# Kernel optimization log

Measured on AMD Instinct MI355X. Metric: run time of the kernel, lower is better.

## Reference

```python
import jax, jax.numpy as jnp
import numpy as np

N = 100_000      # nodes
E = 1_600_000    # edges
EL = 200_000     # labeled edge pairs
NODE_DIM, HID = 32, 256
H2, H4 = HID // 2, HID // 4  # 128, 64


def _lin(k, fan_in, fan_out):
    kw, kb = jax.random.split(k)
    bound = 1.0 / np.sqrt(fan_in)
    W = jax.random.uniform(kw, (fan_in, fan_out), jnp.float32, -bound, bound)
    b = jax.random.uniform(kb, (fan_out,), jnp.float32, -bound, bound)
    return W, b


def setup_inputs() -> dict:
    key = jax.random.key(0)
    ks = jax.random.split(key, 12)
    x = jax.random.normal(ks[0], (N, NODE_DIM), jnp.float32)
    edge_index = jax.random.randint(ks[1], (2, E), 0, N, jnp.int64)
    edge_label_index = jax.random.randint(ks[2], (2, EL), 0, N, jnp.int64)
    enc_w1, enc_b1 = _lin(ks[3], NODE_DIM, HID)
    enc_w2, enc_b2 = _lin(ks[4], HID, H2)
    conv_w0, conv_b0 = _lin(ks[5], H2, H4)
    conv_w1, conv_b1 = _lin(ks[6], H4, H4)
    conv_w2, conv_b2 = _lin(ks[7], H4, H4)
    ep_w1, ep_b1 = _lin(ks[8], 2 * H4, H2)
    ep_w2, ep_b2 = _lin(ks[9], H2, H4)
    ep_w3, ep_b3 = _lin(ks[10], H4, 1)
    return dict(x=x, edge_index=edge_index, edge_label_index=edge_label_index,
                enc_w1=enc_w1, enc_b1=enc_b1, enc_w2=enc_w2, enc_b2=enc_b2,
                conv_w0=conv_w0, conv_b0=conv_b0, conv_w1=conv_w1, conv_b1=conv_b1,
                conv_w2=conv_w2, conv_b2=conv_b2,
                ep_w1=ep_w1, ep_b1=ep_b1, ep_w2=ep_w2, ep_b2=ep_b2, ep_w3=ep_w3, ep_b3=ep_b3)


def reference(x, edge_index, edge_label_index,
              enc_w1, enc_b1, enc_w2, enc_b2,
              conv_w0, conv_b0, conv_w1, conv_b1, conv_w2, conv_b2,
              ep_w1, ep_b1, ep_w2, ep_b2, ep_w3, ep_b3):
    # node encoder (dropout = identity in eval)
    h = jax.nn.relu(x @ enc_w1 + enc_b1)
    h = jax.nn.relu(h @ enc_w2 + enc_b2)           # [N, 128]

    # GCN normalization with self-loops (PyG gcn_norm, edge_weight=1)
    loops = jnp.arange(N, dtype=edge_index.dtype)
    src = jnp.concatenate([edge_index[0], loops])   # [E+N]
    dst = jnp.concatenate([edge_index[1], loops])
    deg = jax.ops.segment_sum(jnp.ones(E + N, jnp.float32), dst, num_segments=N)
    dinv = jnp.where(deg > 0, jax.lax.rsqrt(jnp.maximum(deg, 1.0)), 0.0)
    norm = (dinv[src] * dinv[dst])[:, None]          # [E+N, 1]

    def gcn(h, W, b):
        xw = h @ W                                   # transform first (PyG)
        agg = jax.ops.segment_sum(xw[src] * norm, dst, num_segments=N)
        return agg + b

    for W, b in ((conv_w0, conv_b0), (conv_w1, conv_b1), (conv_w2, conv_b2)):
        h_new = jax.nn.relu(gcn(h, W, b))
        h = h + h_new if h.shape == h_new.shape else h_new
        # self.dropout -> identity in eval

    # edge predictor on labeled pairs
    ef = jnp.concatenate([h[edge_label_index[0]], h[edge_label_index[1]]], axis=1)  # [EL, 128]
    e = jax.nn.relu(ef @ ep_w1 + ep_b1)
    e = jax.nn.relu(e @ ep_w2 + ep_b2)
    e = jax.nn.sigmoid(e @ ep_w3 + ep_b3)
    return e.squeeze(-1)                             # [EL]
```

## Files before the change

kernel.cpp:

```cpp
#include <hip/hip_runtime.h>
#include <math.h>


#define N_NODES 100000
#define N_EDGES 1600000
#define N_EL    200000

#define KBUCK   196
#define WSHIFT  9
#define WMASK   511
#define BCAP    64
#define BSTRIDE 12288
#define PART_NB 512
#define CHUNK   3125
#define LCAP    10240
#define ENC_NB  1563

typedef __attribute__((ext_vector_type(8))) short short8_t;
typedef __attribute__((ext_vector_type(4))) float f32x4;

__device__ __forceinline__ unsigned short f2bf(float f) {
    unsigned u = __float_as_uint(f);
    unsigned r = u + 0x7FFFu + ((u >> 16) & 1u);
    return (unsigned short)(r >> 16);
}

__device__ __forceinline__ float2 up16(unsigned u) {
    union { unsigned v; _Float16 h[2]; } c; c.v = u;
    return make_float2((float)c.h[0], (float)c.h[1]);
}

template<int KTOT, int NTOT>
__device__ __forceinline__ void wprep_one(const float* __restrict__ W, unsigned short* __restrict__ Wp, int flat) {
    if (flat >= KTOT * NTOT) return;
    int j = flat & 7, lane = (flat >> 3) & 63, kstep = (flat >> 9) & 1;
    int rest = flat >> 10;
    int ntile = rest % (NTOT / 16), chunk = rest / (NTOT / 16);
    int k = chunk * 64 + kstep * 32 + (lane >> 4) * 8 + j;
    int n = ntile * 16 + (lane & 15);
    Wp[flat] = f2bf(W[(size_t)k * NTOT + n]);
}

__device__ __forceinline__ void wprep32_one(const float* __restrict__ W, unsigned short* __restrict__ Wp, int flat) {
    if (flat >= 32 * 256) return;
    int j = flat & 7, lane = (flat >> 3) & 63, ntile = flat >> 9;
    int k = (lane >> 4) * 8 + j;
    int n = ntile * 16 + (lane & 15);
    Wp[flat] = f2bf(W[(size_t)k * 256 + n]);
}

__global__ __launch_bounds__(256) void prep0(
    const float* w2, const float* w0, const float* w1, const float* wpp2, const float* w1e,
    const float* wc1, const float* wc2,
    unsigned short* p2, unsigned short* p0, unsigned short* p1, unsigned short* pp2,
    unsigned short* p1e, unsigned short* pc1, unsigned short* pc2,
    int* btail)
{
    int blk = blockIdx.x, t = threadIdx.x;
    if      (blk < 128) wprep_one<256, 128>(w2,  p2,  blk * 256 + t);
    else if (blk < 160) wprep_one<128,  64>(w0,  p0,  (blk - 128) * 256 + t);
    else if (blk < 224) wprep_one<128, 128>(w1,  p1,  (blk - 160) * 256 + t);
    else if (blk < 256) wprep_one<128,  64>(wpp2, pp2, (blk - 224) * 256 + t);
    else if (blk < 288) wprep32_one(w1e, p1e, (blk - 256) * 256 + t);
    else if (blk < 304) wprep_one< 64,  64>(wc1, pc1, (blk - 288) * 256 + t);
    else if (blk < 320) wprep_one< 64,  64>(wc2, pc2, (blk - 304) * 256 + t);
    else                btail[t] = 0;
}

__device__ __forceinline__ void fill_part_body(unsigned char* sm,
                                               const int* __restrict__ ei,
                                               int* __restrict__ btail, int* __restrict__ bscr)
{
    int* base = (int*)sm;
    int (*lbuf)[BCAP] = (int(*)[BCAP])base;
    int* lcnt  = base + 12544;
    int* offs  = base + 12740;
    int* gbase = base + 12937;
    int* sscan = base + 13133;
    int t = threadIdx.x;

    for (int i = t; i < KBUCK; i += 256) lcnt[i] = 0;
    __syncthreads();

    int e0   = blockIdx.x * CHUNK;
    int eend = e0 + CHUNK; if (eend > N_EDGES) eend = N_EDGES;
    for (int e = e0 + t; e < eend; e += 256) {
        int s = __builtin_nontemporal_load(ei + e);
        int d = __builtin_nontemporal_load(ei + N_EDGES + e);
        int b = d >> WSHIFT;
        int entry = ((d & WMASK) << 17) | s;
        int pos = atomicAdd(&lcnt[b], 1);
        if (pos < BCAP) lbuf[b][pos] = entry;
        else {
            int p = atomicAdd(&btail[b], 1);
            bscr[b * BSTRIDE + p] = entry;
        }
    }
    __syncthreads();

    int myc = 0;
    if (t < KBUCK) {
        myc = lcnt[t]; if (myc > BCAP) myc = BCAP;
        lcnt[t] = myc;
        gbase[t] = atomicAdd(&btail[t], myc);
    }
    sscan[t] = (t < KBUCK) ? myc : 0;
    __syncthreads();
    for (int s = 1; s < 256; s <<= 1) {
        int a = (t >= s) ? sscan[t - s] : 0;
        __syncthreads();
        sscan[t] += a;
        __syncthreads();
    }
    if (t < KBUCK) offs[t + 1] = sscan[t];
    if (t == 0) offs[0] = 0;
    __syncthreads();

    int T = offs[KBUCK];
    for (int i = t; i < T; i += 256) {
        int loB = 0, hiB = KBUCK;
        while (hiB - loB > 1) { int mid = (loB + hiB) >> 1; if (offs[mid] <= i) loB = mid; else hiB = mid; }
        int j = i - offs[loB];
        bscr[loB * BSTRIDE + gbase[loB] + j] = lbuf[loB][j];
    }
}

__device__ __forceinline__ void encfull_body(unsigned char* sm, int bid,
    const float* __restrict__ x,
    const unsigned short* __restrict__ Wp1, const float* __restrict__ b1,
    const unsigned short* __restrict__ Wp2, const float* __restrict__ b2,
    const unsigned short* __restrict__ Wp0,
    _Float16* __restrict__ yout, int M)
{
    unsigned short* smem = (unsigned short*)sm;
    unsigned short (*As)[40]   = (unsigned short(*)[40])smem;
    unsigned short* Wls1       = smem + 2560;
    unsigned short (*H1)[264]  = (unsigned short(*)[264])smem;
    unsigned short (*H128)[136]= (unsigned short(*)[136])smem;
    unsigned short* Wls2       = smem + 16896;
    unsigned short* W0s        = smem + 16896;

    int t = threadIdx.x, wave = t >> 6, lane = t & 63;
    int m0 = bid * 64;
    int cb = lane & 15, rq = lane >> 4;

    {
        int row = t >> 2, seg = t & 3;
        int gr = m0 + row;
        float4 a = make_float4(0.f, 0.f, 0.f, 0.f), b = a;
        if (gr < M) {
            a = *(const float4*)&x[(size_t)gr * 32 + seg * 8];
            b = *(const float4*)&x[(size_t)gr * 32 + seg * 8 + 4];
        }
        unsigned short tmp[8] = { f2bf(a.x), f2bf(a.y), f2bf(a.z), f2bf(a.w),
                                  f2bf(b.x), f2bf(b.y), f2bf(b.z), f2bf(b.w) };
        *(uint4*)&As[row][seg * 8] = *(uint4*)tmp;
    }
    #pragma unroll
    for (int j = 0; j < 4; ++j)
        ((uint4*)Wls1)[t + j * 256] = ((const uint4*)Wp1)[t + j * 256];
    __syncthreads();

    short8_t af1 = *(const short8_t*)&As[wave * 16 + cb][rq * 8];
    f32x4 acc[16];
    #pragma unroll
    for (int nt = 0; nt < 16; ++nt) {
        short8_t bf = *(const short8_t*)&Wls1[(nt * 64 + lane) * 8];
        acc[nt] = __builtin_amdgcn_mfma_f32_16x16x32_bf16(af1, bf, (f32x4){0.f, 0.f, 0.f, 0.f}, 0, 0, 0);
    }
    __syncthreads();

    #pragma unroll
    for (int nt = 0; nt < 16; ++nt) {
        int col = nt * 16 + cb;
        float bv = b1[col];
        #pragma unroll
        for (int r = 0; r < 4; ++r)
            H1[wave * 16 + rq * 4 + r][col] = f2bf(fmaxf(acc[nt][r] + bv, 0.f));
    }

    f32x4 acc2[8];
    #pragma unroll
    for (int nt = 0; nt < 8; ++nt) acc2[nt] = (f32x4){0.f, 0.f, 0.f, 0.f};
    for (int ch = 0; ch < 4; ++ch) {
        #pragma unroll
        for (int j = 0; j < 4; ++j)
            ((uint4*)Wls2)[t + j * 256] = ((const uint4*)(Wp2 + (size_t)ch * 8192))[t + j * 256];
        __syncthreads();
        #pragma unroll
        for (int ks = 0; ks < 2; ++ks) {
            short8_t af = *(const short8_t*)&H1[wave * 16 + cb][ch * 64 + ks * 32 + rq * 8];
            #pragma unroll
            for (int nt = 0; nt < 8; ++nt) {
                short8_t bf = *(const short8_t*)&Wls2[((nt * 2 + ks) * 64 + lane) * 8];
                acc2[nt] = __builtin_amdgcn_mfma_f32_16x16x32_bf16(af, bf, acc2[nt], 0, 0, 0);
            }
        }
        __syncthreads();
    }

    #pragma unroll
    for (int nt = 0; nt < 8; ++nt) {
        int col = nt * 16 + cb;
        float bv = b2[col];
        #pragma unroll
        for (int r = 0; r < 4; ++r)
            H128[wave * 16 + rq * 4 + r][col] = f2bf(fmaxf(acc2[nt][r] + bv, 0.f));
    }
    ((uint4*)W0s)[t]       = ((const uint4*)Wp0)[t];
    ((uint4*)W0s)[t + 256] = ((const uint4*)Wp0)[t + 256];
    __syncthreads();

    f32x4 acc3[4];
    #pragma unroll
    for (int nt = 0; nt < 4; ++nt) acc3[nt] = (f32x4){0.f, 0.f, 0.f, 0.f};
    #pragma unroll
    for (int ch = 0; ch < 2; ++ch) {
        #pragma unroll
        for (int ks = 0; ks < 2; ++ks) {
            short8_t af = *(const short8_t*)&H128[wave * 16 + cb][ch * 64 + ks * 32 + rq * 8];
            #pragma unroll
            for (int nt = 0; nt < 4; ++nt) {
                short8_t bf = *(const short8_t*)&W0s[(((ch * 4 + nt) * 2 + ks) * 64 + lane) * 8];
                acc3[nt] = __builtin_amdgcn_mfma_f32_16x16x32_bf16(af, bf, acc3[nt], 0, 0, 0);
            }
        }
    }

    #pragma unroll
    for (int nt = 0; nt < 4; ++nt) {
        int col = nt * 16 + cb;
        #pragma unroll
        for (int r = 0; r < 4; ++r) {
            int gr = m0 + wave * 16 + rq * 4 + r;
            if (gr < M) yout[(size_t)gr * 64 + col] = (_Float16)(acc3[nt][r]);
        }
    }
}

__global__ __launch_bounds__(256, 3) void mega_fill_enc(
    const int* __restrict__ ei, int* __restrict__ btail, int* __restrict__ bscr,
    const float* __restrict__ x,
    const unsigned short* __restrict__ Wp1, const float* __restrict__ b1,
    const unsigned short* __restrict__ Wp2, const float* __restrict__ b2,
    const unsigned short* __restrict__ Wp0,
    _Float16* __restrict__ yout)
{
    __shared__ __align__(16) unsigned char sm[53568];
    if (blockIdx.x < PART_NB)
        fill_part_body(sm, ei, btail, bscr);
    else
        encfull_body(sm, blockIdx.x - PART_NB, x, Wp1, b1, Wp2, b2, Wp0, yout, N_NODES);
}

__global__ __launch_bounds__(512) void fill_place(const int* __restrict__ btail,
                                                  const int* __restrict__ bscr,
                                                  int* __restrict__ row_ptr, float* __restrict__ dinv,
                                                  int* __restrict__ col) {
    __shared__ int ssm[256];
    __shared__ int lcnt[512];
    __shared__ int lpre[512];
    __shared__ int lbuf[LCAP];
    int b = blockIdx.x, t = threadIdx.x;

    if (t < 256) ssm[t] = (t < KBUCK) ? btail[t] : 0;
    lcnt[t] = 0;
    __syncthreads();
    for (int s = 1; s < 256; s <<= 1) {
        int a = 0;
        if (t < 256 && t >= s) a = ssm[t - s];
        __syncthreads();
        if (t < 256) ssm[t] += a;
        __syncthreads();
    }
    int segstart = (b == 0) ? 0 : ssm[b - 1];
    int n = btail[b];
    const int* src = bscr + b * BSTRIDE;
    for (int i = t; i < n; i += 512)
        atomicAdd(&lcnt[src[i] >> 17], 1);
    __syncthreads();

    int c = lcnt[t];
    lpre[t] = c; __syncthreads();
    for (int s = 1; s < 512; s <<= 1) {
        int a = (t >= s) ? lpre[t - s] : 0;
        __syncthreads();
        lpre[t] += a;
        __syncthreads();
    }
    int excl = lpre[t] - c;

    int v = (b << WSHIFT) + t;
    if (v < N_NODES) {
        row_ptr[v] = segstart + excl;
        dinv[v] = rsqrtf((float)(c + 1));
    }
    if (b == KBUCK - 1 && t == 0) row_ptr[N_NODES] = N_EDGES;
    lcnt[t] = excl;
    __syncthreads();

    if (n <= LCAP) {
        for (int i = t; i < n; i += 512) {
            int e = src[i];
            int pos = atomicAdd(&lcnt[e >> 17], 1);
            lbuf[pos] = e & 0x1FFFF;
        }
        __syncthreads();
        for (int i = t; i < n; i += 512)
            col[segstart + i] = lbuf[i];
    } else {
        for (int i = t; i < n; i += 512) {
            int e = src[i];
            int pos = atomicAdd(&lcnt[e >> 17], 1);
            col[segstart + pos] = e & 0x1FFFF;
        }
    }
}

template<bool RESIDUAL, bool EDGE_DINV>
__device__ __forceinline__ void aggcv_body(
    const uint4* __restrict__ y4, const int* __restrict__ row_ptr, const int* __restrict__ col,
    const float* __restrict__ dinv, const float* __restrict__ bias,
    const unsigned short* __restrict__ Wp,
    _Float16* __restrict__ h,
    _Float16* __restrict__ yout)
{
    __shared__ __align__(16) unsigned short Ws[4096];
    __shared__ __align__(16) unsigned short Hs[32][72];
    __shared__ float Dv[32];

    int t = threadIdx.x;
    ((uint4*)Ws)[t]       = ((const uint4*)Wp)[t];
    ((uint4*)Ws)[t + 256] = ((const uint4*)Wp)[t + 256];

    int n  = t >> 3;
    int sl = t & 7;
    int v  = blockIdx.x * 32 + n;

    float dv = dinv[v];

    float s[8];
    {
        uint4 a = y4[(size_t)v * 8 + sl];
        float2 g;
        float w = EDGE_DINV ? dv : 1.0f;
        if (EDGE_DINV) {
            g = up16(a.x); s[0] = w * g.x; s[1] = w * g.y;  g = up16(a.y); s[2] = w * g.x; s[3] = w * g.y;
            g = up16(a.z); s[4] = w * g.x; s[5] = w * g.y;  g = up16(a.w); s[6] = w * g.x; s[7] = w * g.y;
        } else {
            g = up16(a.x); s[0] = g.x; s[1] = g.y;  g = up16(a.y); s[2] = g.x; s[3] = g.y;
            g = up16(a.z); s[4] = g.x; s[5] = g.y;  g = up16(a.w); s[6] = g.x; s[7] = g.y;
        }
    }
    auto accrow = [&](uint4 f, float w) {
        float2 g;
        if (EDGE_DINV) {
            g = up16(f.x); s[0] += w * g.x; s[1] += w * g.y;  g = up16(f.y); s[2] += w * g.x; s[3] += w * g.y;
            g = up16(f.z); s[4] += w * g.x; s[5] += w * g.y;  g = up16(f.w); s[6] += w * g.x; s[7] += w * g.y;
        } else {
            g = up16(f.x); s[0] += g.x; s[1] += g.y;  g = up16(f.y); s[2] += g.x; s[3] += g.y;
            g = up16(f.z); s[4] += g.x; s[5] += g.y;  g = up16(f.w); s[6] += g.x; s[7] += g.y;
        }
    };

    int rs = row_ptr[v], re = row_ptr[v + 1];
    int i = rs;
    for (; i + 7 < re; i += 8) {
        int u0 = col[i],     u1 = col[i + 1], u2 = col[i + 2], u3 = col[i + 3];
        int u4 = col[i + 4], u5 = col[i + 5], u6 = col[i + 6], u7 = col[i + 7];
        float d0 = EDGE_DINV ? dinv[u0] : 1.0f, d1 = EDGE_DINV ? dinv[u1] : 1.0f;
        float d2 = EDGE_DINV ? dinv[u2] : 1.0f, d3 = EDGE_DINV ? dinv[u3] : 1.0f;
        float d4 = EDGE_DINV ? dinv[u4] : 1.0f, d5 = EDGE_DINV ? dinv[u5] : 1.0f;
        float d6 = EDGE_DINV ? dinv[u6] : 1.0f, d7 = EDGE_DINV ? dinv[u7] : 1.0f;
        uint4 f0 = y4[(size_t)u0 * 8 + sl];
        uint4 f1 = y4[(size_t)u1 * 8 + sl];
        uint4 f2 = y4[(size_t)u2 * 8 + sl];
        uint4 f3 = y4[(size_t)u3 * 8 + sl];
        uint4 f4 = y4[(size_t)u4 * 8 + sl];
        uint4 f5 = y4[(size_t)u5 * 8 + sl];
        uint4 f6 = y4[(size_t)u6 * 8 + sl];
        uint4 f7 = y4[(size_t)u7 * 8 + sl];
        accrow(f0, d0); accrow(f1, d1); accrow(f2, d2); accrow(f3, d3);
        accrow(f4, d4); accrow(f5, d5); accrow(f6, d6); accrow(f7, d7);
    }
    for (; i + 3 < re; i += 4) {
        int u0 = col[i], u1 = col[i + 1], u2 = col[i + 2], u3 = col[i + 3];
        float d0 = EDGE_DINV ? dinv[u0] : 1.0f, d1 = EDGE_DINV ? dinv[u1] : 1.0f;
        float d2 = EDGE_DINV ? dinv[u2] : 1.0f, d3 = EDGE_DINV ? dinv[u3] : 1.0f;
        uint4 f0 = y4[(size_t)u0 * 8 + sl];
        uint4 f1 = y4[(size_t)u1 * 8 + sl];
        uint4 f2 = y4[(size_t)u2 * 8 + sl];
        uint4 f3 = y4[(size_t)u3 * 8 + sl];
        accrow(f0, d0); accrow(f1, d1); accrow(f2, d2); accrow(f3, d3);
    }
    for (; i < re; ++i) {
        int u = col[i];
        float d = EDGE_DINV ? dinv[u] : 1.0f;
        accrow(y4[(size_t)u * 8 + sl], d);
    }

    float4 ba = *(const float4*)&bias[sl * 8];
    float4 bb = *(const float4*)&bias[sl * 8 + 4];
    float v0 = fmaxf(dv * s[0] + ba.x, 0.f), v1 = fmaxf(dv * s[1] + ba.y, 0.f);
    float v2 = fmaxf(dv * s[2] + ba.z, 0.f), v3 = fmaxf(dv * s[3] + ba.w, 0.f);
    float v4 = fmaxf(dv * s[4] + bb.x, 0.f), v5 = fmaxf(dv * s[5] + bb.y, 0.f);
    float v6 = fmaxf(dv * s[6] + bb.z, 0.f), v7 = fmaxf(dv * s[7] + bb.w, 0.f);
    if (RESIDUAL) {
        uint4 hr = *(const uint4*)&h[(size_t)v * 64 + sl * 8];
        float2 g;
        g = up16(hr.x); v0 += g.x; v1 += g.y;  g = up16(hr.y); v2 += g.x; v3 += g.y;
        g = up16(hr.z); v4 += g.x; v5 += g.y;  g = up16(hr.w); v6 += g.x; v7 += g.y;
    }
    union { _Float16 hf[8]; uint4 u; } hp;
    hp.hf[0] = (_Float16)v0; hp.hf[1] = (_Float16)v1; hp.hf[2] = (_Float16)v2; hp.hf[3] = (_Float16)v3;
    hp.hf[4] = (_Float16)v4; hp.hf[5] = (_Float16)v5; hp.hf[6] = (_Float16)v6; hp.hf[7] = (_Float16)v7;
    *(uint4*)&h[(size_t)v * 64 + sl * 8] = hp.u;
    union { unsigned short us[8]; uint4 u; } hb;
    hb.us[0] = f2bf(v0); hb.us[1] = f2bf(v1); hb.us[2] = f2bf(v2); hb.us[3] = f2bf(v3);
    hb.us[4] = f2bf(v4); hb.us[5] = f2bf(v5); hb.us[6] = f2bf(v6); hb.us[7] = f2bf(v7);
    *(uint4*)&Hs[n][sl * 8] = hb.u;
    if (sl == 0) Dv[n] = dv;
    __syncthreads();

    int wave = t >> 6, lane = t & 63;
    int rt   = wave & 1;
    int ct0  = (wave >> 1) * 2;
    f32x4 acc0 = (f32x4){0.f, 0.f, 0.f, 0.f}, acc1 = acc0;
    #pragma unroll
    for (int ks = 0; ks < 2; ++ks) {
        short8_t af = *(const short8_t*)&Hs[rt * 16 + (lane & 15)][ks * 32 + (lane >> 4) * 8];
        short8_t b0 = *(const short8_t*)&Ws[((ct0 * 2 + ks) * 64 + lane) * 8];
        short8_t b1 = *(const short8_t*)&Ws[(((ct0 + 1) * 2 + ks) * 64 + lane) * 8];
        acc0 = __builtin_amdgcn_mfma_f32_16x16x32_bf16(af, b0, acc0, 0, 0, 0);
        acc1 = __builtin_amdgcn_mfma_f32_16x16x32_bf16(af, b1, acc1, 0, 0, 0);
    }
    int cb = lane & 15, rq = lane >> 4;
    #pragma unroll
    for (int r = 0; r < 4; ++r) {
        int row = rt * 16 + rq * 4 + r;
        float dv2 = Dv[row];
        size_t go = (size_t)(blockIdx.x * 32 + row) * 64;
        yout[go + ct0 * 16 + cb]       = (_Float16)(acc0[r] * dv2);
        yout[go + (ct0 + 1) * 16 + cb] = (_Float16)(acc1[r] * dv2);
    }
}

__global__ __launch_bounds__(256, 6) void aggcv0_kernel(
    const uint4* y, const int* rp, const int* col, const float* dinv, const float* b,
    const unsigned short* Wp, _Float16* h, _Float16* yout) {
    aggcv_body<false, true>(y, rp, col, dinv, b, Wp, h, yout);
}
__global__ __launch_bounds__(256, 6) void aggcv1_kernel(
    const uint4* y, const int* rp, const int* col, const float* dinv, const float* b,
    const unsigned short* Wp, _Float16* h, _Float16* yout) {
    aggcv_body<true, false>(y, rp, col, dinv, b, Wp, h, yout);
}

__global__ __launch_bounds__(256, 6) void agg2_kernel(
    const uint4* __restrict__ y4, const int* __restrict__ row_ptr, const int* __restrict__ col,
    const float* __restrict__ dinv, const float* __restrict__ bias,
    const _Float16* __restrict__ hprev, uint4* __restrict__ hb4)
{
    int v  = blockIdx.x * 32 + (threadIdx.x >> 3);
    int sl = threadIdx.x & 7;
    if (v >= N_NODES) return;

    float s[8];
    {
        uint4 a = y4[(size_t)v * 8 + sl];
        float2 g;
        g = up16(a.x); s[0] = g.x; s[1] = g.y;  g = up16(a.y); s[2] = g.x; s[3] = g.y;
        g = up16(a.z); s[4] = g.x; s[5] = g.y;  g = up16(a.w); s[6] = g.x; s[7] = g.y;
    }
    auto accrow = [&](uint4 f) {
        float2 g;
        g = up16(f.x); s[0] += g.x; s[1] += g.y;  g = up16(f.y); s[2] += g.x; s[3] += g.y;
        g = up16(f.z); s[4] += g.x; s[5] += g.y;  g = up16(f.w); s[6] += g.x; s[7] += g.y;
    };

    int rs = row_ptr[v], re = row_ptr[v + 1];
    int i = rs;
    for (; i + 7 < re; i += 8) {
        int u0 = col[i],     u1 = col[i + 1], u2 = col[i + 2], u3 = col[i + 3];
        int u4 = col[i + 4], u5 = col[i + 5], u6 = col[i + 6], u7 = col[i + 7];
        uint4 f0 = y4[(size_t)u0 * 8 + sl];
        uint4 f1 = y4[(size_t)u1 * 8 + sl];
        uint4 f2 = y4[(size_t)u2 * 8 + sl];
        uint4 f3 = y4[(size_t)u3 * 8 + sl];
        uint4 f4 = y4[(size_t)u4 * 8 + sl];
        uint4 f5 = y4[(size_t)u5 * 8 + sl];
        uint4 f6 = y4[(size_t)u6 * 8 + sl];
        uint4 f7 = y4[(size_t)u7 * 8 + sl];
        accrow(f0); accrow(f1); accrow(f2); accrow(f3);
        accrow(f4); accrow(f5); accrow(f6); accrow(f7);
    }
    for (; i + 3 < re; i += 4) {
        int u0 = col[i], u1 = col[i + 1], u2 = col[i + 2], u3 = col[i + 3];
        uint4 f0 = y4[(size_t)u0 * 8 + sl];
        uint4 f1 = y4[(size_t)u1 * 8 + sl];
        uint4 f2 = y4[(size_t)u2 * 8 + sl];
        uint4 f3 = y4[(size_t)u3 * 8 + sl];
        accrow(f0); accrow(f1); accrow(f2); accrow(f3);
    }
    for (; i < re; ++i) accrow(y4[(size_t)col[i] * 8 + sl]);

    float dv = dinv[v];
    float4 ba = *(const float4*)&bias[sl * 8];
    float4 bb = *(const float4*)&bias[sl * 8 + 4];
    float v0 = fmaxf(dv * s[0] + ba.x, 0.f), v1 = fmaxf(dv * s[1] + ba.y, 0.f);
    float v2 = fmaxf(dv * s[2] + ba.z, 0.f), v3 = fmaxf(dv * s[3] + ba.w, 0.f);
    float v4 = fmaxf(dv * s[4] + bb.x, 0.f), v5 = fmaxf(dv * s[5] + bb.y, 0.f);
    float v6 = fmaxf(dv * s[6] + bb.z, 0.f), v7 = fmaxf(dv * s[7] + bb.w, 0.f);
    {
        uint4 hr = *(const uint4*)&hprev[(size_t)v * 64 + sl * 8];
        float2 g;
        g = up16(hr.x); v0 += g.x; v1 += g.y;  g = up16(hr.y); v2 += g.x; v3 += g.y;
        g = up16(hr.z); v4 += g.x; v5 += g.y;  g = up16(hr.w); v6 += g.x; v7 += g.y;
    }
    uint4 p;
    p.x = (unsigned)f2bf(v0) | ((unsigned)f2bf(v1) << 16);
    p.y = (unsigned)f2bf(v2) | ((unsigned)f2bf(v3) << 16);
    p.z = (unsigned)f2bf(v4) | ((unsigned)f2bf(v5) << 16);
    p.w = (unsigned)f2bf(v6) | ((unsigned)f2bf(v7) << 16);
    hb4[(size_t)v * 8 + sl] = p;
}

__global__ __launch_bounds__(256, 4) void mfma_ep12(
    const unsigned short* __restrict__ A, const int* __restrict__ gidx,
    const unsigned short* __restrict__ Wp1, const float* __restrict__ b1,
    const unsigned short* __restrict__ Wp2, const float* __restrict__ b2,
    const float* __restrict__ w3, const float* __restrict__ b3,
    float* __restrict__ out, int M)
{
    __shared__ __align__(16) unsigned short smem[12800];
    unsigned short (*As)[72] = (unsigned short(*)[72])smem;
    unsigned short* Wls = smem + 4608;

    int t = threadIdx.x, wave = t >> 6, lane = t & 63;
    int m0 = blockIdx.x * 64;
    int cb = lane & 15, rq = lane >> 4;

    f32x4 acc[8];
    #pragma unroll
    for (int nt = 0; nt < 8; ++nt) acc[nt] = (f32x4){0.f, 0.f, 0.f, 0.f};

    for (int ch = 0; ch < 2; ++ch) {
        #pragma unroll
        for (int j = 0; j < 2; ++j) {
            int idx = t + j * 256;
            int row = idx >> 3, seg = idx & 7;
            int gr = m0 + row;
            uint4 v = make_uint4(0u, 0u, 0u, 0u);
            if (gr < M) {
                int node = (ch == 0) ? gidx[gr] : gidx[N_EL + gr];
                v = *(const uint4*)(A + (size_t)node * 64 + seg * 8);
            }
            *(uint4*)&As[row][seg * 8] = v;
        }
        #pragma unroll
        for (int j = 0; j < 4; ++j) {
            int idx = t + j * 256;
            ((uint4*)Wls)[idx] = ((const uint4*)(Wp1 + (size_t)ch * 8192))[idx];
        }
        __syncthreads();

        #pragma unroll
        for (int ks = 0; ks < 2; ++ks) {
            short8_t af = *(const short8_t*)&As[wave * 16 + cb][ks * 32 + rq * 8];
            #pragma unroll
            for (int nt = 0; nt < 8; ++nt) {
                short8_t bf = *(const short8_t*)&Wls[((nt * 2 + ks) * 64 + lane) * 8];
                acc[nt] = __builtin_amdgcn_mfma_f32_16x16x32_bf16(af, bf, acc[nt], 0, 0, 0);
            }
        }
        __syncthreads();
    }

    unsigned short (*E1)[136] = (unsigned short(*)[136])smem;
    unsigned short* W2s = smem + 8704;
    #pragma unroll
    for (int nt = 0; nt < 8; ++nt) {
        int col = nt * 16 + cb;
        float bv = b1[col];
        #pragma unroll
        for (int r = 0; r < 4; ++r) {
            int row = wave * 16 + rq * 4 + r;
            E1[row][col] = f2bf(fmaxf(acc[nt][r] + bv, 0.f));
        }
    }
    ((uint4*)W2s)[t]       = ((const uint4*)Wp2)[t];
    ((uint4*)W2s)[t + 256] = ((const uint4*)Wp2)[t + 256];
    __syncthreads();

    f32x4 acc2[4];
    #pragma unroll
    for (int nt = 0; nt < 4; ++nt) acc2[nt] = (f32x4){0.f, 0.f, 0.f, 0.f};
    #pragma unroll
    for (int ch = 0; ch < 2; ++ch) {
        #pragma unroll
        for (int ks = 0; ks < 2; ++ks) {
            short8_t af = *(const short8_t*)&E1[wave * 16 + cb][ch * 64 + ks * 32 + rq * 8];
            #pragma unroll
            for (int nt = 0; nt < 4; ++nt) {
                short8_t bf = *(const short8_t*)&W2s[(((ch * 4 + nt) * 2 + ks) * 64 + lane) * 8];
                acc2[nt] = __builtin_amdgcn_mfma_f32_16x16x32_bf16(af, bf, acc2[nt], 0, 0, 0);
            }
        }
    }

    float s0 = 0.f, s1 = 0.f, s2 = 0.f, s3 = 0.f;
    #pragma unroll
    for (int nt = 0; nt < 4; ++nt) {
        int col = nt * 16 + cb;
        float bv = b2[col], wv = w3[col];
        s0 += fmaxf(acc2[nt][0] + bv, 0.f) * wv;
        s1 += fmaxf(acc2[nt][1] + bv, 0.f) * wv;
        s2 += fmaxf(acc2[nt][2] + bv, 0.f) * wv;
        s3 += fmaxf(acc2[nt][3] + bv, 0.f) * wv;
    }
    #pragma unroll
    for (int off = 1; off < 16; off <<= 1) {
        s0 += __shfl_xor(s0, off);
        s1 += __shfl_xor(s1, off);
        s2 += __shfl_xor(s2, off);
        s3 += __shfl_xor(s3, off);
    }
    if (cb == 0) {
        int gr = m0 + wave * 16 + rq * 4;
        if (gr + 3 < M) {
            float bb = b3[0];
            float4 o;
            o.x = 1.f / (1.f + expf(-(s0 + bb)));
            o.y = 1.f / (1.f + expf(-(s1 + bb)));
            o.z = 1.f / (1.f + expf(-(s2 + bb)));
            o.w = 1.f / (1.f + expf(-(s3 + bb)));
            *(float4*)&out[gr] = o;
        }
    }
}

extern "C" void kernel_launch(void* const* d_in, const int* in_sizes, int n_in,
                              void* d_out, int out_size, void* d_ws, size_t ws_size,
                              hipStream_t stream) {
    const float* x       = (const float*)d_in[0];
    const int*   ei      = (const int*)d_in[1];
    const int*   eli     = (const int*)d_in[2];
    const float* enc_w1  = (const float*)d_in[3];
    const float* enc_b1  = (const float*)d_in[4];
    const float* enc_w2  = (const float*)d_in[5];
    const float* enc_b2  = (const float*)d_in[6];
    const float* conv_w0 = (const float*)d_in[7];
    const float* conv_b0 = (const float*)d_in[8];
    const float* conv_w1 = (const float*)d_in[9];
    const float* conv_b1 = (const float*)d_in[10];
    const float* conv_w2 = (const float*)d_in[11];
    const float* conv_b2 = (const float*)d_in[12];
    const float* ep_w1   = (const float*)d_in[13];
    const float* ep_b1   = (const float*)d_in[14];
    const float* ep_w2   = (const float*)d_in[15];
    const float* ep_b2   = (const float*)d_in[16];
    const float* ep_w3   = (const float*)d_in[17];
    const float* ep_b3   = (const float*)d_in[18];
    float* out = (float*)d_out;

    float* fws = (float*)d_ws;
    _Float16* yb         = (_Float16*)fws;
    _Float16* h16        = (_Float16*)(fws + 3200000);
    unsigned short* h64b = (unsigned short*)(fws + 9600000);
    int*   col     = (int*)(fws + 12800000);
    int*   row_ptr = col + 1600000;
    float* dinvp   = (float*)(row_ptr + 100032);
    unsigned short* w2p = (unsigned short*)(dinvp + 100000);
    unsigned short* w0p = w2p + 32768;
    unsigned short* w1p = w0p + 8192;
    unsigned short* wp2 = w1p + 16384;
    unsigned short* w1e = wp2 + 8192;
    unsigned short* wc1p = w1e + 8192;
    unsigned short* wc2p = wc1p + 4096;
    int*   btail   = (int*)(wc2p + 4096);
    int*   bscr    = btail + 256;

    _Float16* yb2 = (_Float16*)h64b;

    const int GBE = N_EL / 64;
    const int GBA = N_NODES / 32;

    prep0<<<321, 256, 0, stream>>>(enc_w2, conv_w0, ep_w1, ep_w2, enc_w1, conv_w1, conv_w2,
                                   w2p, w0p, w1p, wp2, w1e, wc1p, wc2p, btail);

    mega_fill_enc<<<PART_NB + ENC_NB, 256, 0, stream>>>(ei, btail, bscr,
        x, w1e, enc_b1, w2p, enc_b2, w0p, yb);

    fill_place<<<KBUCK, 512, 0, stream>>>(btail, bscr, row_ptr, dinvp, col);

    aggcv0_kernel<<<GBA, 256, 0, stream>>>((const uint4*)yb, row_ptr, col, dinvp, conv_b0,
                                           wc1p, h16, yb2);
    aggcv1_kernel<<<GBA, 256, 0, stream>>>((const uint4*)yb2, row_ptr, col, dinvp, conv_b1,
                                           wc2p, h16, yb);
    agg2_kernel<<<GBA, 256, 0, stream>>>((const uint4*)yb, row_ptr, col, dinvp, conv_b2,
                                         h16, (uint4*)h64b);

    mfma_ep12<<<GBE, 256, 0, stream>>>(h64b, eli, w1p, ep_b1, wp2, ep_b2, ep_w3, ep_b3, out, N_EL);
}
```

Measured before the change: 273.3 us.

## Co-schedule CSR place stage with encoder instead of partition stage

The edge partition step becomes its own kernel, and the CSR placement step (rewritten for 256 threads, two nodes per thread) is fused into the same launch as the node encoder. The placement work now overlaps the encoder instead of the partition work doing so. The longer placement blocks may hide better behind the encoder and the launch count stays the same. The costs are a smaller placement block, which means more per-thread serial work, and a standalone partition kernel that no longer overlaps anything.

```diff
diff --git a/kernel.cpp b/kernel.cpp
--- a/kernel.cpp
+++ b/kernel.cpp
@@ -67,10 +67,10 @@
     else                btail[t] = 0;
 }
 
-__device__ __forceinline__ void fill_part_body(unsigned char* sm,
-                                               const int* __restrict__ ei,
-                                               int* __restrict__ btail, int* __restrict__ bscr)
+__global__ __launch_bounds__(256) void fill_part(const int* __restrict__ ei,
+                                                 int* __restrict__ btail, int* __restrict__ bscr)
 {
+    __shared__ __align__(16) unsigned char sm[53568];
     int* base = (int*)sm;
     int (*lbuf)[BCAP] = (int(*)[BCAP])base;
     int* lcnt  = base + 12544;
@@ -122,6 +122,77 @@
         while (hiB - loB > 1) { int mid = (loB + hiB) >> 1; if (offs[mid] <= i) loB = mid; else hiB = mid; }
         int j = i - offs[loB];
         bscr[loB * BSTRIDE + gbase[loB] + j] = lbuf[loB][j];
+    }
+}
+
+__device__ __forceinline__ void fill_place_body256(unsigned char* sm, int b,
+    const int* __restrict__ btail, const int* __restrict__ bscr,
+    int* __restrict__ row_ptr, float* __restrict__ dinv, int* __restrict__ col)
+{
+    int* base = (int*)sm;
+    int* ssm  = base;
+    int* lcnt = base + 256;
+    int* lpre = base + 768;
+    int* lbuf = base + 1024;
+    int t = threadIdx.x;
+
+    ssm[t] = (t < KBUCK) ? btail[t] : 0;
+    lcnt[t] = 0; lcnt[t + 256] = 0;
+    __syncthreads();
+    for (int s = 1; s < 256; s <<= 1) {
+        int a = (t >= s) ? ssm[t - s] : 0;
+        __syncthreads();
+        ssm[t] += a;
+        __syncthreads();
+    }
+    int segstart = (b == 0) ? 0 : ssm[b - 1];
+    int n = btail[b];
+    const int* src = bscr + b * BSTRIDE;
+    for (int i = t; i < n; i += 256)
+        atomicAdd(&lcnt[src[i] >> 17], 1);
+    __syncthreads();
+
+    int c0 = lcnt[2 * t], c1 = lcnt[2 * t + 1];
+    int cs = c0 + c1;
+    lpre[t] = cs; __syncthreads();
+    for (int s = 1; s < 256; s <<= 1) {
+        int a = (t >= s) ? lpre[t - s] : 0;
+        __syncthreads();
+        lpre[t] += a;
+        __syncthreads();
+    }
+    int exclp = lpre[t] - cs;
+    int excl0 = exclp, excl1 = exclp + c0;
+
+    int v0 = (b << WSHIFT) + 2 * t;
+    if (v0 < N_NODES) {
+        row_ptr[v0] = segstart + excl0;
+        dinv[v0] = rsqrtf((float)(c0 + 1));
+    }
+    if (v0 + 1 < N_NODES) {
+        row_ptr[v0 + 1] = segstart + excl1;
+        dinv[v0 + 1] = rsqrtf((float)(c1 + 1));
+    }
+    if (b == KBUCK - 1 && t == 0) row_ptr[N_NODES] = N_EDGES;
+    lcnt[2 * t] = excl0;
+    lcnt[2 * t + 1] = excl1;
+    __syncthreads();
+
+    if (n <= LCAP) {
+        for (int i = t; i < n; i += 256) {
+            int e = src[i];
+            int pos = atomicAdd(&lcnt[e >> 17], 1);
+            lbuf[pos] = e & 0x1FFFF;
+        }
+        __syncthreads();
+        for (int i = t; i < n; i += 256)
+            col[segstart + i] = lbuf[i];
+    } else {
+        for (int i = t; i < n; i += 256) {
+            int e = src[i];
+            int pos = atomicAdd(&lcnt[e >> 17], 1);
+            col[segstart + pos] = e & 0x1FFFF;
+        }
     }
 }
 
@@ -238,83 +309,20 @@
     }
 }
 
-__global__ __launch_bounds__(256, 3) void mega_fill_enc(
-    const int* __restrict__ ei, int* __restrict__ btail, int* __restrict__ bscr,
+__global__ __launch_bounds__(256, 3) void mega_place_enc(
+    const int* __restrict__ btail, const int* __restrict__ bscr,
+    int* __restrict__ row_ptr, float* __restrict__ dinv, int* __restrict__ col,
     const float* __restrict__ x,
     const unsigned short* __restrict__ Wp1, const float* __restrict__ b1,
     const unsigned short* __restrict__ Wp2, const float* __restrict__ b2,
     const unsigned short* __restrict__ Wp0,
     _Float16* __restrict__ yout)
 {
-    __shared__ __align__(16) unsigned char sm[53568];
-    if (blockIdx.x < PART_NB)
-        fill_part_body(sm, ei, btail, bscr);
+    __shared__ __align__(16) unsigned char sm[50176];
+    if (blockIdx.x < KBUCK)
+        fill_place_body256(sm, blockIdx.x, btail, bscr, row_ptr, dinv, col);
     else
-        encfull_body(sm, blockIdx.x - PART_NB, x, Wp1, b1, Wp2, b2, Wp0, yout, N_NODES);
-}
-
-__global__ __launch_bounds__(512) void fill_place(const int* __restrict__ btail,
-                                                  const int* __restrict__ bscr,
-                                                  int* __restrict__ row_ptr, float* __restrict__ dinv,
-                                                  int* __restrict__ col) {
-    __shared__ int ssm[256];
-    __shared__ int lcnt[512];
-    __shared__ int lpre[512];
-    __shared__ int lbuf[LCAP];
-    int b = blockIdx.x, t = threadIdx.x;
-
-    if (t < 256) ssm[t] = (t < KBUCK) ? btail[t] : 0;
-    lcnt[t] = 0;
-    __syncthreads();
-    for (int s = 1; s < 256; s <<= 1) {
-        int a = 0;
-        if (t < 256 && t >= s) a = ssm[t - s];
-        __syncthreads();
-        if (t < 256) ssm[t] += a;
-        __syncthreads();
-    }
-    int segstart = (b == 0) ? 0 : ssm[b - 1];
-    int n = btail[b];
-    const int* src = bscr + b * BSTRIDE;
-    for (int i = t; i < n; i += 512)
-        atomicAdd(&lcnt[src[i] >> 17], 1);
-    __syncthreads();
-
-    int c = lcnt[t];
-    lpre[t] = c; __syncthreads();
-    for (int s = 1; s < 512; s <<= 1) {
-        int a = (t >= s) ? lpre[t - s] : 0;
-        __syncthreads();
-        lpre[t] += a;
-        __syncthreads();
-    }
-    int excl = lpre[t] - c;
-
-    int v = (b << WSHIFT) + t;
-    if (v < N_NODES) {
-        row_ptr[v] = segstart + excl;
-        dinv[v] = rsqrtf((float)(c + 1));
-    }
-    if (b == KBUCK - 1 && t == 0) row_ptr[N_NODES] = N_EDGES;
-    lcnt[t] = excl;
-    __syncthreads();
-
-    if (n <= LCAP) {
-        for (int i = t; i < n; i += 512) {
-            int e = src[i];
-            int pos = atomicAdd(&lcnt[e >> 17], 1);
-            lbuf[pos] = e & 0x1FFFF;
-        }
-        __syncthreads();
-        for (int i = t; i < n; i += 512)
-            col[segstart + i] = lbuf[i];
-    } else {
-        for (int i = t; i < n; i += 512) {
-            int e = src[i];
-            int pos = atomicAdd(&lcnt[e >> 17], 1);
-            col[segstart + pos] = e & 0x1FFFF;
-        }
-    }
+        encfull_body(sm, blockIdx.x - KBUCK, x, Wp1, b1, Wp2, b2, Wp0, yout, N_NODES);
 }
 
 template<bool RESIDUAL, bool EDGE_DINV>
@@ -688,10 +696,10 @@
     prep0<<<321, 256, 0, stream>>>(enc_w2, conv_w0, ep_w1, ep_w2, enc_w1, conv_w1, conv_w2,
                                    w2p, w0p, w1p, wp2, w1e, wc1p, wc2p, btail);
 
-    mega_fill_enc<<<PART_NB + ENC_NB, 256, 0, stream>>>(ei, btail, bscr,
+    fill_part<<<PART_NB, 256, 0, stream>>>(ei, btail, bscr);
+
+    mega_place_enc<<<KBUCK + ENC_NB, 256, 0, stream>>>(btail, bscr, row_ptr, dinvp, col,
         x, w1e, enc_b1, w2p, enc_b2, w0p, yb);
-
-    fill_place<<<KBUCK, 512, 0, stream>>>(btail, bscr, row_ptr, dinvp, col);
 
     aggcv0_kernel<<<GBA, 256, 0, stream>>>((const uint4*)yb, row_ptr, col, dinvp, conv_b0,
                                            wc1p, h16, yb2);
```

After: 276.5 us. Within noise of the previous version (+1.2%).
